# Kernel tuning notes

Measured on AMD Instinct MI355X. Metric: run time of the kernel, lower is better.

## Reference

```python
import jax, jax.numpy as jnp
import numpy as np

B, S, DIM = 2, 2048, 1024
H, W = 16, 256
HD = DIM // H
SCALE = HD ** -0.5


def setup_inputs() -> dict:
    key = jax.random.key(0)
    ks = jax.random.split(key, 9)
    std = DIM ** -0.5
    return {
        "x": jax.random.normal(ks[0], (B, S, DIM), dtype=jnp.float32),
        "Wq": jax.random.normal(ks[1], (DIM, DIM), dtype=jnp.float32) * std,
        "bq": jnp.zeros((DIM,), dtype=jnp.float32),
        "Wk": jax.random.normal(ks[2], (DIM, DIM), dtype=jnp.float32) * std,
        "bk": jnp.zeros((DIM,), dtype=jnp.float32),
        "Wv": jax.random.normal(ks[3], (DIM, DIM), dtype=jnp.float32) * std,
        "bv": jnp.zeros((DIM,), dtype=jnp.float32),
        "Wo": jax.random.normal(ks[4], (DIM, DIM), dtype=jnp.float32) * std,
        "bo": jnp.zeros((DIM,), dtype=jnp.float32),
    }


def reference(x, Wq, bq, Wk, bk, Wv, bv, Wo, bo):
    b, s, dim = x.shape
    q = (x @ Wq + bq).reshape(b, s, H, HD).transpose(0, 2, 1, 3)  # [B,H,S,HD]
    k = (x @ Wk + bk).reshape(b, s, H, HD).transpose(0, 2, 1, 3)
    v = (x @ Wv + bv).reshape(b, s, H, HD).transpose(0, 2, 1, 3)

    scores = jnp.einsum("bhid,bhjd->bhij", q, k) * SCALE  # [B,H,S,S]
    i = jnp.arange(s)[:, None]
    j = jnp.arange(s)[None, :]
    # valid keys: within causal sliding window [i-W+1, i]
    valid = (j <= i) & (j >= i - W + 1)
    scores = jnp.where(valid, scores, -jnp.inf)
    attn = jax.nn.softmax(scores, axis=-1)
    out = jnp.einsum("bhij,bhjd->bhid", attn, v)  # [B,H,S,HD]
    out = out.transpose(0, 2, 1, 3).reshape(b, s, dim)
    return out @ Wo + bo
```

## Files before the change

### kernel.cpp

```cpp
#include <hip/hip_runtime.h>
#include <stdint.h>

typedef __bf16 bf16;
typedef __bf16 bf16x8 __attribute__((ext_vector_type(8)));
typedef float f32x4 __attribute__((ext_vector_type(4)));

#define MFMA16(a, b, c) __builtin_amdgcn_mfma_f32_16x16x32_bf16((a), (b), (c), 0, 0, 0)

__device__ __forceinline__ void ldsdma16(const void* g, void* l) {
  __builtin_amdgcn_global_load_lds((const __attribute__((address_space(1))) void*)g,
                                   (__attribute__((address_space(3))) void*)l, 16, 0, 0);
}

__global__ __launch_bounds__(256) void prep_cast(const float* __restrict__ x,
                                                 bf16* __restrict__ xb) {
  int idx = (blockIdx.x * 256 + threadIdx.x) * 4;
  float4 v = *(const float4*)(x + idx);
  union { bf16 h[4]; uint2 u; } p;
  p.h[0] = (bf16)v.x; p.h[1] = (bf16)v.y; p.h[2] = (bf16)v.z; p.h[3] = (bf16)v.w;
  *(uint2*)(xb + idx) = p.u;
}

__global__ __launch_bounds__(256) void prep_transpose(const float* __restrict__ Wq,
                                                      const float* __restrict__ Wk,
                                                      const float* __restrict__ Wv,
                                                      const float* __restrict__ Wo,
                                                      bf16* __restrict__ WT) {
  __shared__ float tile[64][65];
  const float* src = blockIdx.z == 0 ? Wq : blockIdx.z == 1 ? Wk : blockIdx.z == 2 ? Wv : Wo;
  bf16* dst = WT + (size_t)blockIdx.z * 1024 * 1024;
  const int k0 = blockIdx.y * 64, n0 = blockIdx.x * 64;
  const int rr = threadIdx.x >> 6, c = threadIdx.x & 63;
#pragma unroll
  for (int i = 0; i < 16; ++i) {
    int r = i * 4 + rr;
    tile[r][c] = src[(size_t)(k0 + r) * 1024 + n0 + c];
  }
  __syncthreads();
#pragma unroll
  for (int i = 0; i < 16; ++i) {
    int r = i * 4 + rr;
    dst[(size_t)(n0 + r) * 1024 + k0 + c] = (bf16)tile[c][r];
  }
}

__device__ __forceinline__ void gemm_mainloop(const bf16* __restrict__ A,
                                              const bf16* __restrict__ BT, int K,
                                              int m0, int n0, bf16* As, bf16* Bs,
                                              f32x4 acc[4][4]) {
  const int tid = threadIdx.x;
  const int lane = tid & 63;
  const int wave = tid >> 6;
  const int wm = wave >> 1, wn = wave & 1;
  const int quad = lane >> 4, l16 = lane & 15;

  const f32x4 zero = {0.f, 0.f, 0.f, 0.f};
#pragma unroll
  for (int i = 0; i < 4; ++i)
#pragma unroll
    for (int j = 0; j < 4; ++j) acc[i][j] = zero;

  const int ch0 = wave * 128 + lane;

  for (int k0 = 0; k0 < K; k0 += 32) {
#pragma unroll
    for (int c = 0; c < 2; ++c) {
      int chunk = ch0 + c * 64;
      int row = chunk >> 2;
      int cg = (chunk & 3) ^ ((row >> 1) & 3);
      ldsdma16(A + (size_t)(m0 + row) * K + k0 + cg * 8,
               (char*)As + (size_t)(wave * 128 + c * 64) * 16);
      ldsdma16(BT + (size_t)(n0 + row) * K + k0 + cg * 8,
               (char*)Bs + (size_t)(wave * 128 + c * 64) * 16);
    }
    __syncthreads();
    bf16x8 af[4], bfv[4];
#pragma unroll
    for (int i = 0; i < 4; ++i) {
      int ra = wm * 64 + i * 16 + l16;
      af[i] = ((const bf16x8*)As)[ra * 4 + (quad ^ ((ra >> 1) & 3))];
      int rb = wn * 64 + i * 16 + l16;
      bfv[i] = ((const bf16x8*)Bs)[rb * 4 + (quad ^ ((rb >> 1) & 3))];
    }
#pragma unroll
    for (int i = 0; i < 4; ++i)
#pragma unroll
      for (int j = 0; j < 4; ++j) acc[i][j] = MFMA16(af[i], bfv[j], acc[i][j]);
    __syncthreads();
  }
}

__global__ __launch_bounds__(256) void qkv_gemm(const bf16* __restrict__ xb,
                                                const bf16* __restrict__ WT,
                                                const float* __restrict__ bq,
                                                const float* __restrict__ bk,
                                                const float* __restrict__ bv,
                                                bf16* __restrict__ Qd,
                                                bf16* __restrict__ Kd,
                                                bf16* __restrict__ Vd) {
  __shared__ bf16 As[128 * 32] __attribute__((aligned(16)));
  __shared__ bf16 Bs[128 * 32] __attribute__((aligned(16)));
  f32x4 acc[4][4];
  const int m0 = blockIdx.y * 128, n0 = blockIdx.x * 128;
  gemm_mainloop(xb, WT, 1024, m0, n0, As, Bs, acc);

  const int lane = threadIdx.x & 63, wave = threadIdx.x >> 6;
  const int wm = wave >> 1, wn = wave & 1;
  const int quad = lane >> 4, l16 = lane & 15;
#pragma unroll
  for (int j = 0; j < 4; ++j) {
    const int n = n0 + wn * 64 + j * 16 + l16;
    const int sel = n >> 10, d = n & 1023;
    const float bias = (sel == 0 ? bq : sel == 1 ? bk : bv)[d];
    bf16* dst = (sel == 0 ? Qd : sel == 1 ? Kd : Vd);
    const float scl = (sel == 0) ? 0.125f : 1.f;
    const int h = d >> 6, hd = d & 63;
#pragma unroll
    for (int i = 0; i < 4; ++i) {
#pragma unroll
      for (int r = 0; r < 4; ++r) {
        const int token = m0 + wm * 64 + i * 16 + quad * 4 + r;
        const int bb = token >> 11, s = token & 2047;
        const float v = (acc[i][j][r] + bias) * scl;
        dst[((((size_t)bb * 16 + h) * 2048 + s) << 6) + hd] = (bf16)v;
      }
    }
  }
}

__global__ __launch_bounds__(256) void attn_kernel(const bf16* __restrict__ Q,
                                                   const bf16* __restrict__ K,
                                                   const bf16* __restrict__ V,
                                                   bf16* __restrict__ Ao) {
  __shared__ bf16 Qs[64 * 64] __attribute__((aligned(16)));
  __shared__ bf16 Ks[64 * 64] __attribute__((aligned(16)));
  __shared__ bf16 Vt[64 * 72] __attribute__((aligned(16)));
  __shared__ bf16 Ps[4][16 * 72] __attribute__((aligned(16)));

  const int tid = threadIdx.x, lane = tid & 63, wave = tid >> 6;
  const int quad = lane >> 4, l16 = lane & 15;
  const int qt = blockIdx.x, h = blockIdx.y, b = blockIdx.z;
  const int q0 = qt * 64;
  const size_t base = ((size_t)(b * 16 + h)) * 2048 * 64;
  const bf16* Qb = Q + base + (size_t)q0 * 64;
  const bf16* Kb = K + base;
  const bf16* Vb = V + base;

#pragma unroll
  for (int c = 0; c < 2; ++c) {
    int chunk = wave * 128 + c * 64 + lane;
    int row = chunk >> 3;
    int cg = (chunk & 7) ^ (row & 7);
    ldsdma16(Qb + (size_t)row * 64 + cg * 8, (char*)Qs + (size_t)(wave * 128 + c * 64) * 16);
  }
  __syncthreads();

  bf16x8 qa[2];
  {
    int row = wave * 16 + l16;
    qa[0] = ((const bf16x8*)Qs)[row * 8 + ((0 * 4 + quad) ^ (row & 7))];
    qa[1] = ((const bf16x8*)Qs)[row * 8 + ((1 * 4 + quad) ^ (row & 7))];
  }

  float mrow[4], lrow[4];
  f32x4 oacc[4];
  const f32x4 zero = {0.f, 0.f, 0.f, 0.f};
#pragma unroll
  for (int r = 0; r < 4; ++r) { mrow[r] = -1e30f; lrow[r] = 0.f; }
#pragma unroll
  for (int t = 0; t < 4; ++t) oacc[t] = zero;

  const int clo = (qt >= 4) ? (qt - 4) : 0;
  for (int ck = clo; ck <= qt; ++ck) {
    const int c0 = ck * 64;
    __syncthreads();
#pragma unroll
    for (int c = 0; c < 2; ++c) {
      int chunk = wave * 128 + c * 64 + lane;
      int row = chunk >> 3;
      int cg = (chunk & 7) ^ (row & 7);
      ldsdma16(Kb + (size_t)(c0 + row) * 64 + cg * 8,
               (char*)Ks + (size_t)(wave * 128 + c * 64) * 16);
    }
    {
      int key = tid >> 2, hc = (tid & 3) * 16;
      const bf16* vp = Vb + (size_t)(c0 + key) * 64 + hc;
      bf16x8 v0 = *(const bf16x8*)vp;
      bf16x8 v1 = *(const bf16x8*)(vp + 8);
#pragma unroll
      for (int i = 0; i < 8; ++i) Vt[(hc + i) * 72 + key] = v0[i];
#pragma unroll
      for (int i = 0; i < 8; ++i) Vt[(hc + 8 + i) * 72 + key] = v1[i];
    }
    __syncthreads();

    f32x4 sc[4];
#pragma unroll
    for (int nt = 0; nt < 4; ++nt) {
      int key = nt * 16 + l16;
      bf16x8 kb0 = ((const bf16x8*)Ks)[key * 8 + ((0 * 4 + quad) ^ (key & 7))];
      bf16x8 kb1 = ((const bf16x8*)Ks)[key * 8 + ((1 * 4 + quad) ^ (key & 7))];
      f32x4 s = zero;
      s = MFMA16(qa[0], kb0, s);
      s = MFMA16(qa[1], kb1, s);
      sc[nt] = s;
    }

    float alpha[4];
#pragma unroll
    for (int r = 0; r < 4; ++r) {
      const int i = q0 + wave * 16 + quad * 4 + r;
      float mx = -1e30f;
#pragma unroll
      for (int nt = 0; nt < 4; ++nt) {
        const int j = c0 + nt * 16 + l16;
        const bool valid = (j <= i) && (j + 255 >= i);
        const float s = valid ? sc[nt][r] : -1e30f;
        sc[nt][r] = s;
        mx = fmaxf(mx, s);
      }
#pragma unroll
      for (int m = 8; m >= 1; m >>= 1) mx = fmaxf(mx, __shfl_xor(mx, m, 64));
      const float mnew = fmaxf(mrow[r], mx);
      alpha[r] = __expf(mrow[r] - mnew);
      mrow[r] = mnew;
      float rs = 0.f;
#pragma unroll
      for (int nt = 0; nt < 4; ++nt) {
        const float p = __expf(sc[nt][r] - mnew);
        sc[nt][r] = p;
        rs += p;
      }
#pragma unroll
      for (int m = 8; m >= 1; m >>= 1) rs += __shfl_xor(rs, m, 64);
      lrow[r] = lrow[r] * alpha[r] + rs;
    }

#pragma unroll
    for (int nt = 0; nt < 4; ++nt)
#pragma unroll
      for (int r = 0; r < 4; ++r)
        Ps[wave][(quad * 4 + r) * 72 + nt * 16 + l16] = (bf16)sc[nt][r];
    asm volatile("s_waitcnt lgkmcnt(0)" ::: "memory");
    bf16x8 pa0 = ((const bf16x8*)Ps[wave])[l16 * 9 + quad];
    bf16x8 pa1 = ((const bf16x8*)Ps[wave])[l16 * 9 + 4 + quad];

#pragma unroll
    for (int ht = 0; ht < 4; ++ht) {
      f32x4 o = oacc[ht];
#pragma unroll
      for (int r = 0; r < 4; ++r) o[r] *= alpha[r];
      const int n = ht * 16 + l16;
      bf16x8 vb0 = ((const bf16x8*)Vt)[n * 9 + quad];
      bf16x8 vb1 = ((const bf16x8*)Vt)[n * 9 + 4 + quad];
      o = MFMA16(pa0, vb0, o);
      o = MFMA16(pa1, vb1, o);
      oacc[ht] = o;
    }
  }

#pragma unroll
  for (int r = 0; r < 4; ++r) {
    const float inv = 1.f / lrow[r];
    const int row = q0 + wave * 16 + quad * 4 + r;
    const size_t outb = ((size_t)(b * 2048 + row)) * 1024 + h * 64;
#pragma unroll
    for (int ht = 0; ht < 4; ++ht)
      Ao[outb + ht * 16 + l16] = (bf16)(oacc[ht][r] * inv);
  }
}

__global__ __launch_bounds__(256) void out_gemm(const bf16* __restrict__ Ain,
                                                const bf16* __restrict__ WoT,
                                                const float* __restrict__ bo,
                                                float* __restrict__ out) {
  __shared__ bf16 As[128 * 32] __attribute__((aligned(16)));
  __shared__ bf16 Bs[128 * 32] __attribute__((aligned(16)));
  f32x4 acc[4][4];
  const int m0 = blockIdx.y * 128, n0 = blockIdx.x * 128;
  gemm_mainloop(Ain, WoT, 1024, m0, n0, As, Bs, acc);

  const int lane = threadIdx.x & 63, wave = threadIdx.x >> 6;
  const int wm = wave >> 1, wn = wave & 1;
  const int quad = lane >> 4, l16 = lane & 15;
#pragma unroll
  for (int j = 0; j < 4; ++j) {
    const int n = n0 + wn * 64 + j * 16 + l16;
    const float bias = bo[n];
#pragma unroll
    for (int i = 0; i < 4; ++i) {
#pragma unroll
      for (int r = 0; r < 4; ++r) {
        const int token = m0 + wm * 64 + i * 16 + quad * 4 + r;
        out[(size_t)token * 1024 + n] = acc[i][j][r] + bias;
      }
    }
  }
}

extern "C" void kernel_launch(void* const* d_in, const int* in_sizes, int n_in,
                              void* d_out, int out_size, void* d_ws, size_t ws_size,
                              hipStream_t stream) {
  const float* x  = (const float*)d_in[0];
  const float* Wq = (const float*)d_in[1];
  const float* bq = (const float*)d_in[2];
  const float* Wk = (const float*)d_in[3];
  const float* bk = (const float*)d_in[4];
  const float* Wv = (const float*)d_in[5];
  const float* bv = (const float*)d_in[6];
  const float* Wo = (const float*)d_in[7];
  const float* bo = (const float*)d_in[8];
  float* out = (float*)d_out;

  char* ws = (char*)d_ws;
  bf16* xb = (bf16*)(ws);
  bf16* WT = (bf16*)(ws + ((size_t)8 << 20));
  bf16* Qd = (bf16*)(ws + ((size_t)16 << 20));
  bf16* Kd = (bf16*)(ws + ((size_t)24 << 20));
  bf16* Vd = (bf16*)(ws + ((size_t)32 << 20));
  bf16* Ao = (bf16*)(ws + ((size_t)40 << 20));

  prep_cast<<<4096, 256, 0, stream>>>(x, xb);
  prep_transpose<<<dim3(16, 16, 4), 256, 0, stream>>>(Wq, Wk, Wv, Wo, WT);
  qkv_gemm<<<dim3(24, 32), 256, 0, stream>>>(xb, WT, bq, bk, bv, Qd, Kd, Vd);
  attn_kernel<<<dim3(32, 16, 2), 256, 0, stream>>>(Qd, Kd, Vd, Ao);
  out_gemm<<<dim3(8, 32), 256, 0, stream>>>(Ao, WT + (size_t)3 * 1024 * 1024, bo, out);
}
```

Before: 173.4 us.

## Fuse prep kernels, pre-transpose V, simplify attention softmax, shrink output GEMM tile

Merges the x cast and the weight transpose into one launch. The QKV GEMM epilogue now writes V transposed, so the attention kernel can load K and V fragments straight from global memory without LDS staging or block barriers. Attention drops the running-max softmax and exponentiates raw scores, applying the window masks only on the edge chunks and reducing row sums once at the end. The output GEMM uses 128x64 tiles to launch more blocks. Skipping max subtraction assumes scores stay small enough that exp cannot overflow. The strided transposed V stores in the QKV epilogue may also cost extra write bandwidth.

```diff
diff --git a/kernel.cpp b/kernel.cpp
--- a/kernel.cpp
+++ b/kernel.cpp
@@ -12,20 +12,25 @@
                                    (__attribute__((address_space(3))) void*)l, 16, 0, 0);
 }
 
-__global__ __launch_bounds__(256) void prep_cast(const float* __restrict__ x,
-                                                 bf16* __restrict__ xb) {
-  int idx = (blockIdx.x * 256 + threadIdx.x) * 4;
-  float4 v = *(const float4*)(x + idx);
-  union { bf16 h[4]; uint2 u; } p;
-  p.h[0] = (bf16)v.x; p.h[1] = (bf16)v.y; p.h[2] = (bf16)v.z; p.h[3] = (bf16)v.w;
-  *(uint2*)(xb + idx) = p.u;
-}
-
-__global__ __launch_bounds__(256) void prep_transpose(const float* __restrict__ Wq,
-                                                      const float* __restrict__ Wk,
-                                                      const float* __restrict__ Wv,
-                                                      const float* __restrict__ Wo,
-                                                      bf16* __restrict__ WT) {
+__global__ __launch_bounds__(256) void prep_kernel(const float* __restrict__ x,
+                                                   const float* __restrict__ Wq,
+                                                   const float* __restrict__ Wk,
+                                                   const float* __restrict__ Wv,
+                                                   const float* __restrict__ Wo,
+                                                   bf16* __restrict__ WT,
+                                                   bf16* __restrict__ xb) {
+  if (blockIdx.z == 4) {
+    const int t = (blockIdx.y * 16 + blockIdx.x) * 256 + threadIdx.x;
+#pragma unroll
+    for (int it = 0; it < 16; ++it) {
+      const int idx = (it * 65536 + t) * 4;
+      float4 v = *(const float4*)(x + idx);
+      union { bf16 h[4]; uint2 u; } p;
+      p.h[0] = (bf16)v.x; p.h[1] = (bf16)v.y; p.h[2] = (bf16)v.z; p.h[3] = (bf16)v.w;
+      *(uint2*)(xb + idx) = p.u;
+    }
+    return;
+  }
   __shared__ float tile[64][65];
   const float* src = blockIdx.z == 0 ? Wq : blockIdx.z == 1 ? Wk : blockIdx.z == 2 ? Wv : Wo;
   bf16* dst = WT + (size_t)blockIdx.z * 1024 * 1024;
@@ -97,7 +102,7 @@
                                                 const float* __restrict__ bv,
                                                 bf16* __restrict__ Qd,
                                                 bf16* __restrict__ Kd,
-                                                bf16* __restrict__ Vd) {
+                                                bf16* __restrict__ Vt) {
   __shared__ bf16 As[128 * 32] __attribute__((aligned(16)));
   __shared__ bf16 Bs[128 * 32] __attribute__((aligned(16)));
   f32x4 acc[4][4];
@@ -112,7 +117,6 @@
     const int n = n0 + wn * 64 + j * 16 + l16;
     const int sel = n >> 10, d = n & 1023;
     const float bias = (sel == 0 ? bq : sel == 1 ? bk : bv)[d];
-    bf16* dst = (sel == 0 ? Qd : sel == 1 ? Kd : Vd);
     const float scl = (sel == 0) ? 0.125f : 1.f;
     const int h = d >> 6, hd = d & 63;
 #pragma unroll
@@ -122,7 +126,12 @@
         const int token = m0 + wm * 64 + i * 16 + quad * 4 + r;
         const int bb = token >> 11, s = token & 2047;
         const float v = (acc[i][j][r] + bias) * scl;
-        dst[((((size_t)bb * 16 + h) * 2048 + s) << 6) + hd] = (bf16)v;
+        if (sel == 2) {
+          Vt[((((size_t)bb * 16 + h) * 64 + hd) << 11) + s] = (bf16)v;
+        } else {
+          bf16* dst = (sel == 0) ? Qd : Kd;
+          dst[((((size_t)bb * 16 + h) * 2048 + s) << 6) + hd] = (bf16)v;
+        }
       }
     }
   }
@@ -130,11 +139,8 @@
 
 __global__ __launch_bounds__(256) void attn_kernel(const bf16* __restrict__ Q,
                                                    const bf16* __restrict__ K,
-                                                   const bf16* __restrict__ V,
+                                                   const bf16* __restrict__ Vt,
                                                    bf16* __restrict__ Ao) {
-  __shared__ bf16 Qs[64 * 64] __attribute__((aligned(16)));
-  __shared__ bf16 Ks[64 * 64] __attribute__((aligned(16)));
-  __shared__ bf16 Vt[64 * 72] __attribute__((aligned(16)));
   __shared__ bf16 Ps[4][16 * 72] __attribute__((aligned(16)));
 
   const int tid = threadIdx.x, lane = tid & 63, wave = tid >> 6;
@@ -144,96 +150,68 @@
   const size_t base = ((size_t)(b * 16 + h)) * 2048 * 64;
   const bf16* Qb = Q + base + (size_t)q0 * 64;
   const bf16* Kb = K + base;
-  const bf16* Vb = V + base;
-
-#pragma unroll
-  for (int c = 0; c < 2; ++c) {
-    int chunk = wave * 128 + c * 64 + lane;
-    int row = chunk >> 3;
-    int cg = (chunk & 7) ^ (row & 7);
-    ldsdma16(Qb + (size_t)row * 64 + cg * 8, (char*)Qs + (size_t)(wave * 128 + c * 64) * 16);
-  }
-  __syncthreads();
-
-  bf16x8 qa[2];
-  {
-    int row = wave * 16 + l16;
-    qa[0] = ((const bf16x8*)Qs)[row * 8 + ((0 * 4 + quad) ^ (row & 7))];
-    qa[1] = ((const bf16x8*)Qs)[row * 8 + ((1 * 4 + quad) ^ (row & 7))];
-  }
-
-  float mrow[4], lrow[4];
+  const bf16* Vb = Vt + base;
+
+  const int qrow = wave * 16 + l16;
+  const bf16x8 qa0 = *(const bf16x8*)(Qb + (size_t)qrow * 64 + quad * 8);
+  const bf16x8 qa1 = *(const bf16x8*)(Qb + (size_t)qrow * 64 + 32 + quad * 8);
+
+  float lrow[4];
   f32x4 oacc[4];
   const f32x4 zero = {0.f, 0.f, 0.f, 0.f};
 #pragma unroll
-  for (int r = 0; r < 4; ++r) { mrow[r] = -1e30f; lrow[r] = 0.f; }
+  for (int r = 0; r < 4; ++r) lrow[r] = 0.f;
 #pragma unroll
   for (int t = 0; t < 4; ++t) oacc[t] = zero;
 
   const int clo = (qt >= 4) ? (qt - 4) : 0;
   for (int ck = clo; ck <= qt; ++ck) {
     const int c0 = ck * 64;
-    __syncthreads();
-#pragma unroll
-    for (int c = 0; c < 2; ++c) {
-      int chunk = wave * 128 + c * 64 + lane;
-      int row = chunk >> 3;
-      int cg = (chunk & 7) ^ (row & 7);
-      ldsdma16(Kb + (size_t)(c0 + row) * 64 + cg * 8,
-               (char*)Ks + (size_t)(wave * 128 + c * 64) * 16);
-    }
-    {
-      int key = tid >> 2, hc = (tid & 3) * 16;
-      const bf16* vp = Vb + (size_t)(c0 + key) * 64 + hc;
-      bf16x8 v0 = *(const bf16x8*)vp;
-      bf16x8 v1 = *(const bf16x8*)(vp + 8);
-#pragma unroll
-      for (int i = 0; i < 8; ++i) Vt[(hc + i) * 72 + key] = v0[i];
-#pragma unroll
-      for (int i = 0; i < 8; ++i) Vt[(hc + 8 + i) * 72 + key] = v1[i];
-    }
-    __syncthreads();
 
     f32x4 sc[4];
 #pragma unroll
     for (int nt = 0; nt < 4; ++nt) {
-      int key = nt * 16 + l16;
-      bf16x8 kb0 = ((const bf16x8*)Ks)[key * 8 + ((0 * 4 + quad) ^ (key & 7))];
-      bf16x8 kb1 = ((const bf16x8*)Ks)[key * 8 + ((1 * 4 + quad) ^ (key & 7))];
-      f32x4 s = zero;
-      s = MFMA16(qa[0], kb0, s);
-      s = MFMA16(qa[1], kb1, s);
-      sc[nt] = s;
-    }
-
-    float alpha[4];
-#pragma unroll
-    for (int r = 0; r < 4; ++r) {
-      const int i = q0 + wave * 16 + quad * 4 + r;
-      float mx = -1e30f;
-#pragma unroll
-      for (int nt = 0; nt < 4; ++nt) {
-        const int j = c0 + nt * 16 + l16;
-        const bool valid = (j <= i) && (j + 255 >= i);
-        const float s = valid ? sc[nt][r] : -1e30f;
-        sc[nt][r] = s;
-        mx = fmaxf(mx, s);
-      }
-#pragma unroll
-      for (int m = 8; m >= 1; m >>= 1) mx = fmaxf(mx, __shfl_xor(mx, m, 64));
-      const float mnew = fmaxf(mrow[r], mx);
-      alpha[r] = __expf(mrow[r] - mnew);
-      mrow[r] = mnew;
-      float rs = 0.f;
-#pragma unroll
-      for (int nt = 0; nt < 4; ++nt) {
-        const float p = __expf(sc[nt][r] - mnew);
-        sc[nt][r] = p;
-        rs += p;
-      }
-#pragma unroll
-      for (int m = 8; m >= 1; m >>= 1) rs += __shfl_xor(rs, m, 64);
-      lrow[r] = lrow[r] * alpha[r] + rs;
+      const bf16* kp = Kb + (size_t)(c0 + nt * 16 + l16) * 64 + quad * 8;
+      bf16x8 kb0 = *(const bf16x8*)kp;
+      bf16x8 kb1 = *(const bf16x8*)(kp + 32);
+      f32x4 s = MFMA16(qa0, kb0, zero);
+      sc[nt] = MFMA16(qa1, kb1, s);
+    }
+
+    if (ck == qt) {
+#pragma unroll
+      for (int r = 0; r < 4; ++r) {
+        const int i = q0 + wave * 16 + quad * 4 + r;
+#pragma unroll
+        for (int nt = 0; nt < 4; ++nt) {
+          const int j = c0 + nt * 16 + l16;
+          const float p = (j <= i) ? __expf(sc[nt][r]) : 0.f;
+          sc[nt][r] = p;
+          lrow[r] += p;
+        }
+      }
+    } else if (qt >= 4 && ck == qt - 4) {
+#pragma unroll
+      for (int r = 0; r < 4; ++r) {
+        const int i = q0 + wave * 16 + quad * 4 + r;
+#pragma unroll
+        for (int nt = 0; nt < 4; ++nt) {
+          const int j = c0 + nt * 16 + l16;
+          const float p = (j + 255 >= i) ? __expf(sc[nt][r]) : 0.f;
+          sc[nt][r] = p;
+          lrow[r] += p;
+        }
+      }
+    } else {
+#pragma unroll
+      for (int r = 0; r < 4; ++r) {
+#pragma unroll
+        for (int nt = 0; nt < 4; ++nt) {
+          const float p = __expf(sc[nt][r]);
+          sc[nt][r] = p;
+          lrow[r] += p;
+        }
+      }
     }
 
 #pragma unroll
@@ -247,20 +225,18 @@
 
 #pragma unroll
     for (int ht = 0; ht < 4; ++ht) {
-      f32x4 o = oacc[ht];
-#pragma unroll
-      for (int r = 0; r < 4; ++r) o[r] *= alpha[r];
-      const int n = ht * 16 + l16;
-      bf16x8 vb0 = ((const bf16x8*)Vt)[n * 9 + quad];
-      bf16x8 vb1 = ((const bf16x8*)Vt)[n * 9 + 4 + quad];
-      o = MFMA16(pa0, vb0, o);
-      o = MFMA16(pa1, vb1, o);
-      oacc[ht] = o;
+      const bf16* vp = Vb + (size_t)(ht * 16 + l16) * 2048 + c0 + quad * 8;
+      bf16x8 vb0 = *(const bf16x8*)vp;
+      bf16x8 vb1 = *(const bf16x8*)(vp + 32);
+      f32x4 o = MFMA16(pa0, vb0, oacc[ht]);
+      oacc[ht] = MFMA16(pa1, vb1, o);
     }
   }
 
 #pragma unroll
   for (int r = 0; r < 4; ++r) {
+#pragma unroll
+    for (int m = 8; m >= 1; m >>= 1) lrow[r] += __shfl_xor(lrow[r], m, 64);
     const float inv = 1.f / lrow[r];
     const int row = q0 + wave * 16 + quad * 4 + r;
     const size_t outb = ((size_t)(b * 2048 + row)) * 1024 + h * 64;
@@ -275,17 +251,57 @@
                                                 const float* __restrict__ bo,
                                                 float* __restrict__ out) {
   __shared__ bf16 As[128 * 32] __attribute__((aligned(16)));
-  __shared__ bf16 Bs[128 * 32] __attribute__((aligned(16)));
-  f32x4 acc[4][4];
-  const int m0 = blockIdx.y * 128, n0 = blockIdx.x * 128;
-  gemm_mainloop(Ain, WoT, 1024, m0, n0, As, Bs, acc);
-
-  const int lane = threadIdx.x & 63, wave = threadIdx.x >> 6;
+  __shared__ bf16 Bs[64 * 32] __attribute__((aligned(16)));
+  const int tid = threadIdx.x, lane = tid & 63, wave = tid >> 6;
   const int wm = wave >> 1, wn = wave & 1;
   const int quad = lane >> 4, l16 = lane & 15;
-#pragma unroll
-  for (int j = 0; j < 4; ++j) {
-    const int n = n0 + wn * 64 + j * 16 + l16;
+  const int m0 = blockIdx.y * 128, n0 = blockIdx.x * 64;
+
+  f32x4 acc[4][2];
+  const f32x4 zero = {0.f, 0.f, 0.f, 0.f};
+#pragma unroll
+  for (int i = 0; i < 4; ++i)
+#pragma unroll
+    for (int j = 0; j < 2; ++j) acc[i][j] = zero;
+
+  for (int k0 = 0; k0 < 1024; k0 += 32) {
+#pragma unroll
+    for (int c = 0; c < 2; ++c) {
+      int chunk = wave * 64 + c * 256 + lane;
+      int row = chunk >> 2;
+      int cg = (chunk & 3) ^ ((row >> 1) & 3);
+      ldsdma16(Ain + (size_t)(m0 + row) * 1024 + k0 + cg * 8,
+               (char*)As + (size_t)(wave * 64 + c * 256) * 16);
+    }
+    {
+      int chunk = wave * 64 + lane;
+      int row = chunk >> 2;
+      int cg = (chunk & 3) ^ ((row >> 1) & 3);
+      ldsdma16(WoT + (size_t)(n0 + row) * 1024 + k0 + cg * 8,
+               (char*)Bs + (size_t)(wave * 64) * 16);
+    }
+    __syncthreads();
+    bf16x8 af[4], bfv[2];
+#pragma unroll
+    for (int i = 0; i < 4; ++i) {
+      int ra = wm * 64 + i * 16 + l16;
+      af[i] = ((const bf16x8*)As)[ra * 4 + (quad ^ ((ra >> 1) & 3))];
+    }
+#pragma unroll
+    for (int j = 0; j < 2; ++j) {
+      int rb = wn * 32 + j * 16 + l16;
+      bfv[j] = ((const bf16x8*)Bs)[rb * 4 + (quad ^ ((rb >> 1) & 3))];
+    }
+#pragma unroll
+    for (int i = 0; i < 4; ++i)
+#pragma unroll
+      for (int j = 0; j < 2; ++j) acc[i][j] = MFMA16(af[i], bfv[j], acc[i][j]);
+    __syncthreads();
+  }
+
+#pragma unroll
+  for (int j = 0; j < 2; ++j) {
+    const int n = n0 + wn * 32 + j * 16 + l16;
     const float bias = bo[n];
 #pragma unroll
     for (int i = 0; i < 4; ++i) {
@@ -317,12 +333,11 @@
   bf16* WT = (bf16*)(ws + ((size_t)8 << 20));
   bf16* Qd = (bf16*)(ws + ((size_t)16 << 20));
   bf16* Kd = (bf16*)(ws + ((size_t)24 << 20));
-  bf16* Vd = (bf16*)(ws + ((size_t)32 << 20));
+  bf16* Vt = (bf16*)(ws + ((size_t)32 << 20));
   bf16* Ao = (bf16*)(ws + ((size_t)40 << 20));
 
-  prep_cast<<<4096, 256, 0, stream>>>(x, xb);
-  prep_transpose<<<dim3(16, 16, 4), 256, 0, stream>>>(Wq, Wk, Wv, Wo, WT);
-  qkv_gemm<<<dim3(24, 32), 256, 0, stream>>>(xb, WT, bq, bk, bv, Qd, Kd, Vd);
-  attn_kernel<<<dim3(32, 16, 2), 256, 0, stream>>>(Qd, Kd, Vd, Ao);
-  out_gemm<<<dim3(8, 32), 256, 0, stream>>>(Ao, WT + (size_t)3 * 1024 * 1024, bo, out);
-}
+  prep_kernel<<<dim3(16, 16, 5), 256, 0, stream>>>(x, Wq, Wk, Wv, Wo, WT, xb);
+  qkv_gemm<<<dim3(24, 32), 256, 0, stream>>>(xb, WT, bq, bk, bv, Qd, Kd, Vt);
+  attn_kernel<<<dim3(32, 16, 2), 256, 0, stream>>>(Qd, Kd, Vt, Ao);
+  out_gemm<<<dim3(16, 32), 256, 0, stream>>>(Ao, WT + (size_t)3 * 1024 * 1024, bo, out);
+}
```

After: 190.4 us. 9.8% more time.
